# Kernel optimization log

Hardware: AMD Instinct MI355X
Metric: run time of the kernel (lower is better)

The kernel has to match this reference:

```python
import jax, jax.numpy as jnp
import numpy as np


def setup_inputs() -> dict:
    key = jax.random.key(0)
    k1, k2 = jax.random.split(key)
    B, S, H, K = 128, 128, 128, 8
    inputs = jax.random.normal(k1, (B, S, H), dtype=jnp.float32)
    threshes = jax.random.uniform(k2, (K,), dtype=jnp.float32)
    return {"inputs": inputs, "threshes": threshes}


def reference(inputs, threshes):
    # Faithful translation of the torch triple loop:
    # a single (B,) accumulator is carried sequentially over
    # (time i, hidden j, neuron k) in row-major order; x[:, i, j] is
    # re-added at every neuron step (first-ever assignment == add to 0).
    B, S, H = inputs.shape
    K = threshes.shape[0]
    x_flat = inputs.reshape(B, S * H).T  # (T, B) with T = S*H

    def outer(s, x_t):  # one (i, j) step
        def inner(s, th):  # one neuron step k
            s = s + x_t
            spike = s > th
            out = jnp.where(spike, s, jnp.zeros((), s.dtype))  # spike * acc
            s = s - out  # reset where spiked
            return s, (out, spike)
        s, (outs, spikes) = jax.lax.scan(inner, s, threshes)  # (K, B)
        return s, (outs, spikes)

    s0 = jnp.zeros((B,), inputs.dtype)
    _, (outs, spikes) = jax.lax.scan(outer, s0, x_flat)  # (T, K, B)

    # (T, K, B) -> (B, S, K, H): torch stacks neurons at dim=1, hidden at dim=2,
    # time at dim=1 of the final stack -> final layout (batch, seq, K, hidden).
    outs = outs.transpose(2, 0, 1).reshape(B, S, H, K).transpose(0, 1, 3, 2)
    spikes = spikes.transpose(2, 0, 1).reshape(B, S, H, K).transpose(0, 1, 3, 2)
    return outs, spikes
```

## Files before the change

### kernel.cpp

```cpp
#include <hip/hip_runtime.h>
#include <math.h>


#define NB 128
#define NS 128
#define NH 128
#define NK 8
#define NT (NS * NH)
#define WL 8
#define NW2 (NT / WL)
#define NG64 (NT / 64)
#define NP64 (NW2 / 64)
#define OUTN ((size_t)NB * NS * NK * NH)

#define WS_M     0
#define WS_M64   (NB * NW2)
#define WS_SENT  (NB * NW2 + NB * NG64)
#define WS_TOTAL (2 * NB * NW2 + NB * NG64)

__global__ void lif_bounds(const float* __restrict__ x,
                           const float* __restrict__ th,
                           float* __restrict__ M, float* __restrict__ M64)
{
    int idx = blockIdx.x * 256 + threadIdx.x;
    if (idx >= NB * NG64) return;
    int b = idx >> 8, gg = idx & (NG64 - 1);
    float t[NK];
#pragma unroll
    for (int k = 0; k < NK; ++k) t[k] = th[k];
    const float* xp = x + (size_t)b * NT + gg * 64;

    double pg = 0.0, gmax = -1e300;
#pragma unroll
    for (int w8 = 0; w8 < 8; ++w8) {
        double pw = 0.0, wmax = -1e300;
#pragma unroll
        for (int l = 0; l < 8; ++l) {
            double xv = (double)xp[w8 * 8 + l];
#pragma unroll
            for (int k = 0; k < NK; ++k) {
                pw += xv;
                double rel = pw - (double)t[k];
                wmax = fmax(wmax, rel);
            }
        }
        gmax = fmax(gmax, pg + wmax);
        pg += pw;
        M[(size_t)b * NW2 + gg * 8 + w8] =
            (float)(-wmax - 0.1 - 1e-6 * fabs(wmax));
    }
    M64[(size_t)b * NG64 + gg] = (float)(-gmax - 0.5 - 1e-6 * fabs(gmax));
}

#define ADD8(xv) do { s += xv; s += xv; s += xv; s += xv; \
                      s += xv; s += xv; s += xv; s += xv; } while (0)
#define STEP8(xv) do { \
    s += xv; s = (s > th0) ? 0.0f : s; \
    s += xv; s = (s > th1) ? 0.0f : s; \
    s += xv; s = (s > th2) ? 0.0f : s; \
    s += xv; s = (s > th3) ? 0.0f : s; \
    s += xv; s = (s > th4) ? 0.0f : s; \
    s += xv; s = (s > th5) ? 0.0f : s; \
    s += xv; s = (s > th6) ? 0.0f : s; \
    s += xv; s = (s > th7) ? 0.0f : s; } while (0)

__device__ __forceinline__ float rl(float v, int idx) {
    return __int_as_float(__builtin_amdgcn_readlane(__float_as_int(v), idx));
}

__global__ void __launch_bounds__(64, 1)
lif_chain(const float* __restrict__ x, const float* __restrict__ th,
          const float* __restrict__ M, const float* __restrict__ M64,
          float* __restrict__ s_ent)
{
    const int b = blockIdx.x;
    const int lane = threadIdx.x;
    const float* xb   = x + (size_t)b * NT;
    const float* Mb   = M + (size_t)b * NW2;
    const float* M64b = M64 + (size_t)b * NG64;
    float* seb = s_ent + (size_t)b * NW2;

    const float th0 = th[0], th1 = th[1], th2 = th[2], th3 = th[3];
    const float th4 = th[4], th5 = th[5], th6 = th[6], th7 = th[7];

    float s = 0.0f, keep = 0.0f;
    float cx   = xb[lane];
    float cM   = Mb[lane];
    float cM64 = M64b[0];

    for (int p = 0; p < NP64; ++p) {
        float nM = Mb[(size_t)((p + 1 < NP64) ? p + 1 : p) * 64 + lane];
        for (int g8 = 0; g8 < 8; ++g8) {
            const int gg = p * 8 + g8;
            const int ggn = (gg + 1 < NG64) ? gg + 1 : gg;
            float nx   = xb[(size_t)ggn * 64 + lane];
            float nM64 = M64b[ggn];
            const int wbase = g8 * 8;

            int q64 = __builtin_amdgcn_readfirstlane((int)(s <= cM64));
            if (q64) {
                float xc = rl(cx, 0);
#pragma unroll
                for (int wi = 0; wi < 8; ++wi) {
                    keep = (lane == wbase + wi) ? s : keep;
#pragma unroll
                    for (int m = 0; m < 8; ++m) {
                        int ni = wi * 8 + m + 1; if (ni > 63) ni = 63;
                        float xn = rl(cx, ni);
                        ADD8(xc);
                        xc = xn;
                    }
                }
            } else {
#pragma unroll
                for (int wi = 0; wi < 8; ++wi) {
                    float Mc = rl(cM, wbase + wi);
                    keep = (lane == wbase + wi) ? s : keep;
                    float xc = rl(cx, wi * 8);
                    int q = __builtin_amdgcn_readfirstlane((int)(s <= Mc));
                    if (q) {
#pragma unroll
                        for (int m = 0; m < 8; ++m) {
                            int ni = wi * 8 + m + 1; if (ni > 63) ni = 63;
                            float xn = rl(cx, ni);
                            ADD8(xc);
                            xc = xn;
                        }
                    } else {
#pragma unroll
                        for (int m = 0; m < 8; ++m) {
                            int ni = wi * 8 + m + 1; if (ni > 63) ni = 63;
                            float xn = rl(cx, ni);
                            STEP8(xc);
                            xc = xn;
                        }
                    }
                }
            }
            cx = nx; cM64 = nM64;
        }
        seb[(size_t)p * 64 + lane] = keep;
        cM = nM;
    }
}

__global__ void __launch_bounds__(128)
lif_out(const float* __restrict__ x, const float* __restrict__ th,
        const float* __restrict__ s_ent, float* __restrict__ out)
{
    const int j = threadIdx.x;
    const int i = blockIdx.x & (NS - 1);
    const int b = blockIdx.x >> 7;
    const int wl = j >> 3;
    const int r  = j & 7;

    const float th0 = th[0], th1 = th[1], th2 = th[2], th3 = th[3];
    const float th4 = th[4], th5 = th[5], th6 = th[6], th7 = th[7];

    float s = s_ent[(size_t)b * NW2 + i * 16 + wl];
    const float* xrow = x + (size_t)b * NT + i * NH + (wl << 3);

    for (int m = 0; m < r; ++m) {
        float xv = xrow[m];
        STEP8(xv);
    }
    float xv = xrow[r];

    float* o  = out + (((size_t)b * NS + i) * NK) * NH + j;
    float* sp = o + OUTN;
    float thr[NK];
#pragma unroll
    for (int k = 0; k < NK; ++k) thr[k] = th[k];
#pragma unroll
    for (int k = 0; k < NK; ++k) {
        s += xv;
        bool spike = s > thr[k];
        o[(size_t)k * NH]  = spike ? s : 0.0f;
        sp[(size_t)k * NH] = spike ? 1.0f : 0.0f;
        s = spike ? 0.0f : s;
    }
}

__global__ void lif_mono(const float* __restrict__ x, const float* __restrict__ th,
                         float* __restrict__ out)
{
    int b = blockIdx.x * 64 + threadIdx.x;
    if (b >= NB) return;
    float thr[NK];
#pragma unroll
    for (int k = 0; k < NK; ++k) thr[k] = th[k];
    const float* xb = x + (size_t)b * NT;
    float s = 0.0f;
    for (int i = 0; i < NS; ++i)
        for (int j = 0; j < NH; ++j) {
            float xv = xb[i * NH + j];
#pragma unroll
            for (int k = 0; k < NK; ++k) {
                s += xv;
                bool spike = s > thr[k];
                size_t idx = (((size_t)b * NS + i) * NK + k) * NH + j;
                out[idx]        = spike ? s : 0.0f;
                out[OUTN + idx] = spike ? 1.0f : 0.0f;
                s = spike ? 0.0f : s;
            }
        }
}

extern "C" void kernel_launch(void* const* d_in, const int* in_sizes, int n_in,
                              void* d_out, int out_size, void* d_ws, size_t ws_size,
                              hipStream_t stream) {
    const float* x  = (const float*)d_in[0];
    const float* th = (const float*)d_in[1];
    float* out = (float*)d_out;

    if (ws_size >= (size_t)WS_TOTAL * sizeof(float)) {
        float* ws    = (float*)d_ws;
        float* Mbuf  = ws + WS_M;
        float* M64b  = ws + WS_M64;
        float* s_ent = ws + WS_SENT;

        lif_bounds<<<dim3((NB * NG64 + 255) / 256), dim3(256), 0, stream>>>(x, th, Mbuf, M64b);
        lif_chain<<<dim3(NB), dim3(64), 0, stream>>>(x, th, Mbuf, M64b, s_ent);
        lif_out<<<dim3(NB * NS), dim3(128), 0, stream>>>(x, th, s_ent, out);
    } else {
        lif_mono<<<dim3(2), dim3(64), 0, stream>>>(x, th, out);
    }
}
```

Baseline: 417.2 us.

## Replace per-window step chain with precomputed reset-interval lookup tables

Adds a precompute kernel that, for each 8-element window, finds the sequence of record-minimum reset points and stores for each an interval [lo,hi] and the exact end state after that reset. The sequential chain kernel then uses ballots over these intervals to jump straight to the stored end state when the entry state falls safely in one interval, and runs the full step loop only in ambiguous cases. The goal is to shorten the serial per-batch dependency chain, which dominates runtime. In exchange there is an extra table kernel, more workspace traffic, and a correctness risk from the float margin heuristics (MW=0.08) that only hold approximately.

```diff
diff --git a/kernel.cpp b/kernel.cpp
--- a/kernel.cpp
+++ b/kernel.cpp
@@ -13,43 +13,15 @@
 #define NP64 (NW2 / 64)
 #define OUTN ((size_t)NB * NS * NK * NH)
 
-#define WS_M     0
-#define WS_M64   (NB * NW2)
-#define WS_SENT  (NB * NW2 + NB * NG64)
-#define WS_TOTAL (2 * NB * NW2 + NB * NG64)
-
-__global__ void lif_bounds(const float* __restrict__ x,
-                           const float* __restrict__ th,
-                           float* __restrict__ M, float* __restrict__ M64)
-{
-    int idx = blockIdx.x * 256 + threadIdx.x;
-    if (idx >= NB * NG64) return;
-    int b = idx >> 8, gg = idx & (NG64 - 1);
-    float t[NK];
-#pragma unroll
-    for (int k = 0; k < NK; ++k) t[k] = th[k];
-    const float* xp = x + (size_t)b * NT + gg * 64;
-
-    double pg = 0.0, gmax = -1e300;
-#pragma unroll
-    for (int w8 = 0; w8 < 8; ++w8) {
-        double pw = 0.0, wmax = -1e300;
-#pragma unroll
-        for (int l = 0; l < 8; ++l) {
-            double xv = (double)xp[w8 * 8 + l];
-#pragma unroll
-            for (int k = 0; k < NK; ++k) {
-                pw += xv;
-                double rel = pw - (double)t[k];
-                wmax = fmax(wmax, rel);
-            }
-        }
-        gmax = fmax(gmax, pg + wmax);
-        pg += pw;
-        M[(size_t)b * NW2 + gg * 8 + w8] =
-            (float)(-wmax - 0.1 - 1e-6 * fabs(wmax));
-    }
-    M64[(size_t)b * NG64 + gg] = (float)(-gmax - 0.5 - 1e-6 * fabs(gmax));
+#define WS_SENT 0
+#define WS_PHI  (NB * NW2)
+#define WS_PLO  (WS_PHI + NB * NG64 * 64)
+#define WS_PK   (WS_PLO + NB * NG64 * 64)
+#define WS_G    (WS_PK  + NB * NG64 * 64)
+#define WS_TOT  (WS_G + NB * NG64)
+
+__device__ __forceinline__ float rl(float v, int idx) {
+    return __int_as_float(__builtin_amdgcn_readlane(__float_as_int(v), idx));
 }
 
 #define ADD8(xv) do { s += xv; s += xv; s += xv; s += xv; \
@@ -64,83 +36,160 @@
     s += xv; s = (s > th6) ? 0.0f : s; \
     s += xv; s = (s > th7) ? 0.0f : s; } while (0)
 
-__device__ __forceinline__ float rl(float v, int idx) {
-    return __int_as_float(__builtin_amdgcn_readlane(__float_as_int(v), idx));
+__global__ void __launch_bounds__(256)
+lif_tab2(const float* __restrict__ x, const float* __restrict__ th,
+         float* __restrict__ PHI, float* __restrict__ PLO,
+         float* __restrict__ PK)
+{
+    int idx = blockIdx.x * 256 + threadIdx.x;
+    if (idx >= NB * NW2) return;
+    int b = idx >> 11, w = idx & (NW2 - 1);
+    int gg = w >> 3, wi = w & 7;
+    const float* xw = x + (size_t)b * NT + w * WL;
+    float t[NK];
+#pragma unroll
+    for (int k = 0; k < NK; ++k) t[k] = th[k];
+
+    double p = 0.0, rmin = 1e300;
+    double rv[7]; int rj[7]; int nr = 0; int over = 0;
+    for (int ss = 0; ss < 64; ++ss) {
+        p += (double)xw[ss >> 3];
+        double m = (double)t[ss & 7] - p;
+        if (m < rmin) {
+            rmin = m;
+            if (nr < 7) { rv[nr] = m; rj[nr] = ss; ++nr; }
+            else over = 1;
+        }
+    }
+    const double MW = 0.08;
+    float hi[8], lo[8], kk[8];
+#pragma unroll
+    for (int i = 0; i < 8; ++i) { hi[i] = 3e38f; lo[i] = 3e38f; kk[i] = 0.0f; }
+    for (int i = 0; i < nr; ++i) {
+        double g = MW + 1e-6 * fabs(rv[i]);
+        hi[i] = (float)(rv[i] + g);
+        lo[i] = (float)(rv[i] - g);
+        float s2 = 0.0f;
+        for (int ss = rj[i] + 1; ss < 64; ++ss) {
+            s2 += xw[ss >> 3];
+            s2 = (s2 > t[ss & 7]) ? 0.0f : s2;
+        }
+        kk[i] = s2;
+    }
+    if (over) {
+        double g = MW + 1e-6 * fabs(rmin);
+        hi[7] = 3e38f;
+        lo[7] = (float)(rmin - g);
+        kk[7] = 0.0f;
+    }
+    size_t base = ((size_t)b * NG64 + gg) * 64 + wi * 8;
+#pragma unroll
+    for (int i = 0; i < 8; ++i) {
+        PHI[base + i] = hi[i]; PLO[base + i] = lo[i]; PK[base + i] = kk[i];
+    }
+}
+
+__global__ void __launch_bounds__(256)
+lif_tabg(const float* __restrict__ x, const float* __restrict__ th,
+         float* __restrict__ G)
+{
+    int idx = blockIdx.x * 256 + threadIdx.x;
+    if (idx >= NB * NG64) return;
+    int b = idx >> 8, gg = idx & (NG64 - 1);
+    const float* xg = x + (size_t)b * NT + gg * 64;
+    float t[NK];
+#pragma unroll
+    for (int k = 0; k < NK; ++k) t[k] = th[k];
+    double p = 0.0, minm = 1e300;
+    for (int ti = 0; ti < 64; ++ti) {
+        double xv = (double)xg[ti];
+#pragma unroll
+        for (int k = 0; k < NK; ++k) {
+            p += xv;
+            double m = (double)t[k] - p;
+            minm = fmin(minm, m);
+        }
+    }
+    G[idx] = (float)(minm - 0.6 - 1e-6 * fabs(minm));
 }
 
 __global__ void __launch_bounds__(64, 1)
-lif_chain(const float* __restrict__ x, const float* __restrict__ th,
-          const float* __restrict__ M, const float* __restrict__ M64,
-          float* __restrict__ s_ent)
+lif_chain_s(const float* __restrict__ x, const float* __restrict__ th,
+            const float* __restrict__ PHI, const float* __restrict__ PLO,
+            const float* __restrict__ PK, const float* __restrict__ Gb_,
+            float* __restrict__ s_ent)
 {
     const int b = blockIdx.x;
     const int lane = threadIdx.x;
     const float* xb   = x + (size_t)b * NT;
-    const float* Mb   = M + (size_t)b * NW2;
-    const float* M64b = M64 + (size_t)b * NG64;
+    const float* PHIb = PHI + (size_t)b * NG64 * 64;
+    const float* PLOb = PLO + (size_t)b * NG64 * 64;
+    const float* PKb  = PK  + (size_t)b * NG64 * 64;
+    const float* Gb   = Gb_ + (size_t)b * NG64;
     float* seb = s_ent + (size_t)b * NW2;
 
     const float th0 = th[0], th1 = th[1], th2 = th[2], th3 = th[3];
     const float th4 = th[4], th5 = th[5], th6 = th[6], th7 = th[7];
 
     float s = 0.0f, keep = 0.0f;
-    float cx   = xb[lane];
-    float cM   = Mb[lane];
-    float cM64 = M64b[0];
+    float cHi = PHIb[lane], cLo = PLOb[lane], cK = PKb[lane];
+    float cx  = xb[lane],   cG  = Gb[0];
 
     for (int p = 0; p < NP64; ++p) {
-        float nM = Mb[(size_t)((p + 1 < NP64) ? p + 1 : p) * 64 + lane];
         for (int g8 = 0; g8 < 8; ++g8) {
             const int gg = p * 8 + g8;
             const int ggn = (gg + 1 < NG64) ? gg + 1 : gg;
-            float nx   = xb[(size_t)ggn * 64 + lane];
-            float nM64 = M64b[ggn];
+            float nHi = PHIb[(size_t)ggn * 64 + lane];
+            float nLo = PLOb[(size_t)ggn * 64 + lane];
+            float nK  = PKb[(size_t)ggn * 64 + lane];
+            float nx  = xb[(size_t)ggn * 64 + lane];
+            float nG  = Gb[ggn];
             const int wbase = g8 * 8;
 
-            int q64 = __builtin_amdgcn_readfirstlane((int)(s <= cM64));
+            int q64 = __builtin_amdgcn_readfirstlane((int)(s <= cG));
             if (q64) {
-                float xc = rl(cx, 0);
 #pragma unroll
                 for (int wi = 0; wi < 8; ++wi) {
                     keep = (lane == wbase + wi) ? s : keep;
 #pragma unroll
                     for (int m = 0; m < 8; ++m) {
-                        int ni = wi * 8 + m + 1; if (ni > 63) ni = 63;
-                        float xn = rl(cx, ni);
+                        float xc = rl(cx, wi * 8 + m);
                         ADD8(xc);
-                        xc = xn;
                     }
                 }
             } else {
 #pragma unroll
                 for (int wi = 0; wi < 8; ++wi) {
-                    float Mc = rl(cM, wbase + wi);
                     keep = (lane == wbase + wi) ? s : keep;
-                    float xc = rl(cx, wi * 8);
-                    int q = __builtin_amdgcn_readfirstlane((int)(s <= Mc));
-                    if (q) {
-#pragma unroll
-                        for (int m = 0; m < 8; ++m) {
-                            int ni = wi * 8 + m + 1; if (ni > 63) ni = 63;
-                            float xn = rl(cx, ni);
-                            ADD8(xc);
-                            xc = xn;
+                    unsigned long long bHi = __ballot(s > cHi);
+                    unsigned long long bLo = __ballot(s > cLo);
+                    unsigned hi8 = (unsigned)(bHi >> (wi * 8)) & 0xffu;
+                    unsigned lo8 = (unsigned)(bLo >> (wi * 8)) & 0xffu;
+                    int ii = __ffs((int)hi8);
+                    unsigned below = ii ? (lo8 & ((1u << (ii - 1)) - 1u))
+                                        : lo8;
+                    if (below == 0) {
+                        if (ii) {
+                            s = rl(cK, wi * 8 + ii - 1);
+                        } else {
+#pragma unroll
+                            for (int m = 0; m < 8; ++m) {
+                                float xc = rl(cx, wi * 8 + m);
+                                ADD8(xc);
+                            }
                         }
                     } else {
 #pragma unroll
                         for (int m = 0; m < 8; ++m) {
-                            int ni = wi * 8 + m + 1; if (ni > 63) ni = 63;
-                            float xn = rl(cx, ni);
+                            float xc = rl(cx, wi * 8 + m);
                             STEP8(xc);
-                            xc = xn;
                         }
                     }
                 }
             }
-            cx = nx; cM64 = nM64;
+            cHi = nHi; cLo = nLo; cK = nK; cx = nx; cG = nG;
         }
         seb[(size_t)p * 64 + lane] = keep;
-        cM = nM;
     }
 }
 
@@ -212,15 +261,18 @@
     const float* x  = (const float*)d_in[0];
     const float* th = (const float*)d_in[1];
     float* out = (float*)d_out;
-
-    if (ws_size >= (size_t)WS_TOTAL * sizeof(float)) {
-        float* ws    = (float*)d_ws;
-        float* Mbuf  = ws + WS_M;
-        float* M64b  = ws + WS_M64;
+    float* ws  = (float*)d_ws;
+
+    if (ws_size >= (size_t)WS_TOT * sizeof(float)) {
         float* s_ent = ws + WS_SENT;
-
-        lif_bounds<<<dim3((NB * NG64 + 255) / 256), dim3(256), 0, stream>>>(x, th, Mbuf, M64b);
-        lif_chain<<<dim3(NB), dim3(64), 0, stream>>>(x, th, Mbuf, M64b, s_ent);
+        float* PHI   = ws + WS_PHI;
+        float* PLO   = ws + WS_PLO;
+        float* PK    = ws + WS_PK;
+        float* G     = ws + WS_G;
+
+        lif_tab2<<<dim3((NB * NW2 + 255) / 256), dim3(256), 0, stream>>>(x, th, PHI, PLO, PK);
+        lif_tabg<<<dim3((NB * NG64 + 255) / 256), dim3(256), 0, stream>>>(x, th, G);
+        lif_chain_s<<<dim3(NB), dim3(64), 0, stream>>>(x, th, PHI, PLO, PK, G, s_ent);
         lif_out<<<dim3(NB * NS), dim3(128), 0, stream>>>(x, th, s_ent, out);
     } else {
         lif_mono<<<dim3(2), dim3(64), 0, stream>>>(x, th, out);
```

Measured after the change: 583.6 us. 1.4x slower.
